# Optimization experiments

Measured on AMD Instinct MI355X. Metric: run time of the kernel, lower is better.

The kernel has to match this reference:

```python
import jax, jax.numpy as jnp
import numpy as np

N_NODES = 50000
N_EDGES = 800000
D_IN = 96
D_OUT = 96
N_GRAPHS = 50


def setup_inputs() -> dict:
    key = jax.random.key(0)
    ks = jax.random.split(key, 16)
    s = 1.0 / np.sqrt(D_IN)
    inp = {
        "x": jax.random.normal(ks[0], (N_NODES, D_IN), jnp.float32),
        "edge_index": jax.random.randint(ks[1], (2, N_EDGES), 0, N_NODES, jnp.int32),
        "edge_attr": jax.random.uniform(ks[2], (N_EDGES, 1), jnp.float32),
        "batch": jnp.sort(jax.random.randint(ks[3], (N_NODES,), 0, N_GRAPHS, jnp.int32)),
        "w1_w": jax.random.normal(ks[4], (D_IN, D_OUT), jnp.float32) * s,
        "w1_b": jax.random.normal(ks[5], (D_OUT,), jnp.float32) * 0.01,
        "w2_w": jax.random.normal(ks[6], (D_IN, D_OUT), jnp.float32) * s,
        "w2_b": jax.random.normal(ks[7], (D_OUT,), jnp.float32) * 0.01,
        "w3_w": jax.random.normal(ks[8], (D_IN, D_OUT), jnp.float32) * s,
        "w3_b": jax.random.normal(ks[9], (D_OUT,), jnp.float32) * 0.01,
        "w4_w": jax.random.normal(ks[10], (D_IN, D_OUT), jnp.float32) * s,
        "w4_b": jax.random.normal(ks[11], (D_OUT,), jnp.float32) * 0.01,
        "w5_w": jax.random.normal(ks[12], (1, D_OUT), jnp.float32),
        "w5_b": jax.random.normal(ks[13], (D_OUT,), jnp.float32) * 0.01,
    }
    return inp


def reference(x, edge_index, edge_attr, batch,
              w1_w, w1_b, w2_w, w2_b, w3_w, w3_b, w4_w, w4_b, w5_w, w5_b):
    n = x.shape[0]
    src, dst = edge_index[0], edge_index[1]  # x_j = x[src], x_i = x[dst]
    sqrt_d = jnp.sqrt(jnp.asarray(D_OUT, x.dtype))

    x_i = x[dst]                                  # [E, D]
    x_j = x[src]                                  # [E, D]
    xi_t = x_i @ w3_w + w3_b                      # w3(x_i)
    xj_t = x_j @ w4_w + w4_b                      # w4(x_j)
    ea_t = edge_attr @ w5_w + w5_b                # w5(edge_attr), [E, D]

    scores = jnp.sum(xi_t * (xj_t + ea_t), axis=-1) / sqrt_d  # [E]

    # segment softmax over destination-node neighborhoods (PyG softmax)
    seg_max = jax.ops.segment_max(scores, dst, num_segments=n)
    ex = jnp.exp(scores - seg_max[dst])
    denom = jax.ops.segment_sum(ex, dst, num_segments=n)
    alpha = ex / (denom[dst] + jnp.asarray(1e-16, x.dtype))

    msg = alpha[:, None] * (x_j @ w2_w + w2_b)    # [E, D]
    aggr = jax.ops.segment_sum(msg, dst, num_segments=n)

    node_out = x @ w1_w + w1_b + aggr             # update: w1(x) + aggr

    # global mean pool per graph
    sums = jax.ops.segment_sum(node_out, batch, num_segments=N_GRAPHS)
    counts = jax.ops.segment_sum(jnp.ones((n,), x.dtype), batch, num_segments=N_GRAPHS)
    return sums / jnp.maximum(counts, 1.0)[:, None]
```

## Files before the change

### kernel.cpp

```cpp
#include <hip/hip_runtime.h>
#include <math.h>

#define D 96
#define RSQ 0.10206207261596577f
#define TSTRIDE 104

typedef __attribute__((ext_vector_type(8))) short short8;
typedef __attribute__((ext_vector_type(4))) float f32x4;

__device__ __forceinline__ unsigned short f2bf(float f){
  unsigned u = __float_as_uint(f);
  unsigned r = (u + 0x7fff + ((u >> 16) & 1)) >> 16;
  return (unsigned short)r;
}
__device__ __forceinline__ float bf2f(unsigned short h){
  return __uint_as_float(((unsigned)h) << 16);
}
__device__ __forceinline__ float bflo(unsigned u){ return __uint_as_float(u << 16); }
__device__ __forceinline__ float bfhi(unsigned u){ return __uint_as_float(u & 0xffff0000u); }
__device__ __forceinline__ int lbound(const int* __restrict__ a, int n, int v){
  int lo = 0, hi = n;
  while (lo < hi){ int mid = (lo + hi) >> 1; if (a[mid] < v) lo = mid + 1; else hi = mid; }
  return lo;
}

__global__ __launch_bounds__(256) void k_wprep(
    const float* __restrict__ w1, const float* __restrict__ w2,
    const float* __restrict__ w3, const float* __restrict__ w4,
    unsigned short* __restrict__ wt_h, unsigned short* __restrict__ wt_l){
  int idx = blockIdx.x * 256 + threadIdx.x;
  if (idx >= 4 * D * D) return;
  int m = idx / (D * D);
  int r = idx % (D * D);
  int nn = r / D, k = r % D;
  const float* w = (m == 0) ? w1 : (m == 1) ? w2 : (m == 2) ? w3 : w4;
  float v = w[k * D + nn];
  unsigned short h = f2bf(v);
  wt_h[idx] = h;
  wt_l[idx] = f2bf(v - bf2f(h));
}

__global__ __launch_bounds__(256) void k_transform_mfma(
    const float* __restrict__ x,
    const unsigned short* __restrict__ wt_h, const unsigned short* __restrict__ wt_l,
    const float* __restrict__ b1, const float* __restrict__ b2,
    const float* __restrict__ b3, const float* __restrict__ b4,
    const float* __restrict__ w5, const float* __restrict__ b5,
    float* __restrict__ acc_o, unsigned short* __restrict__ x2o,
    float* __restrict__ x3o, unsigned short* __restrict__ x4o,
    float* __restrict__ p5, float* __restrict__ pb, int n){
  __shared__ __align__(16) unsigned short xs_h[16][TSTRIDE];
  __shared__ __align__(16) unsigned short xs_l[16][TSTRIDE];
  int tid = threadIdx.x;
  int n0 = blockIdx.x * 16;
  for (int e = tid; e < 16 * D; e += 256){
    int r = e / D, c = e % D;
    int node = n0 + r;
    float v = (node < n) ? x[(size_t)node * D + c] : 0.0f;
    unsigned short h = f2bf(v);
    xs_h[r][c] = h;
    xs_l[r][c] = f2bf(v - bf2f(h));
  }
  __syncthreads();

  int wv = tid >> 6;
  int lane = tid & 63;
  int lr = lane & 15;
  int kg = lane >> 4;

  f32x4 acc0 = {0,0,0,0}, acc1 = {0,0,0,0}, acc2 = {0,0,0,0};
  f32x4 acc3 = {0,0,0,0}, acc4 = {0,0,0,0}, acc5 = {0,0,0,0};
  const unsigned short* wtm_h = wt_h + (size_t)wv * D * D;
  const unsigned short* wtm_l = wt_l + (size_t)wv * D * D;

  #pragma unroll
  for (int k0 = 0; k0 < D; k0 += 32){
    int kb = k0 + kg * 8;
    short8 ah = *(const short8*)&xs_h[lr][kb];
    short8 al = *(const short8*)&xs_l[lr][kb];
    #pragma unroll
    for (int nc = 0; nc < 6; ++nc){
      int col = nc * 16 + lr;
      short8 bh = *(const short8*)(wtm_h + col * D + kb);
      short8 bl = *(const short8*)(wtm_l + col * D + kb);
      f32x4 a = (nc == 0) ? acc0 : (nc == 1) ? acc1 : (nc == 2) ? acc2
              : (nc == 3) ? acc3 : (nc == 4) ? acc4 : acc5;
      a = __builtin_amdgcn_mfma_f32_16x16x32_bf16(ah, bh, a, 0, 0, 0);
      a = __builtin_amdgcn_mfma_f32_16x16x32_bf16(ah, bl, a, 0, 0, 0);
      a = __builtin_amdgcn_mfma_f32_16x16x32_bf16(al, bh, a, 0, 0, 0);
      if (nc == 0) acc0 = a; else if (nc == 1) acc1 = a; else if (nc == 2) acc2 = a;
      else if (nc == 3) acc3 = a; else if (nc == 4) acc4 = a; else acc5 = a;
    }
  }

  const float* bias = (wv == 0) ? b1 : (wv == 1) ? b2 : (wv == 2) ? b3 : b4;
  float p5p0 = 0, p5p1 = 0, p5p2 = 0, p5p3 = 0;
  float pbp0 = 0, pbp1 = 0, pbp2 = 0, pbp3 = 0;
  #pragma unroll
  for (int nc = 0; nc < 6; ++nc){
    int col = nc * 16 + lr;
    float bb = bias[col];
    float w5v = w5[col], b5v = b5[col];
    f32x4 a = (nc == 0) ? acc0 : (nc == 1) ? acc1 : (nc == 2) ? acc2
            : (nc == 3) ? acc3 : (nc == 4) ? acc4 : acc5;
    #pragma unroll
    for (int q = 0; q < 4; ++q){
      float v = a[q] + bb;
      int row = kg * 4 + q;
      if (n0 + row < n){
        size_t o = (size_t)(n0 + row) * D + col;
        if (wv == 0) acc_o[o] = v;
        else if (wv == 1) x2o[o] = f2bf(v);
        else if (wv == 2) x3o[o] = v;
        else x4o[o] = f2bf(v);
      }
      float t5 = v * w5v, tb = v * b5v;
      if (q == 0){ p5p0 += t5; pbp0 += tb; }
      else if (q == 1){ p5p1 += t5; pbp1 += tb; }
      else if (q == 2){ p5p2 += t5; pbp2 += tb; }
      else { p5p3 += t5; pbp3 += tb; }
    }
  }
  if (wv == 2){
    #pragma unroll
    for (int off = 1; off < 16; off <<= 1){
      p5p0 += __shfl_xor(p5p0, off); pbp0 += __shfl_xor(pbp0, off);
      p5p1 += __shfl_xor(p5p1, off); pbp1 += __shfl_xor(pbp1, off);
      p5p2 += __shfl_xor(p5p2, off); pbp2 += __shfl_xor(pbp2, off);
      p5p3 += __shfl_xor(p5p3, off); pbp3 += __shfl_xor(pbp3, off);
    }
    if (lr == 0){
      int row = kg * 4;
      if (n0 + row < n)     { p5[n0 + row]     = p5p0; pb[n0 + row]     = pbp0; }
      if (n0 + row + 1 < n) { p5[n0 + row + 1] = p5p1; pb[n0 + row + 1] = pbp1; }
      if (n0 + row + 2 < n) { p5[n0 + row + 2] = p5p2; pb[n0 + row + 2] = pbp2; }
      if (n0 + row + 3 < n) { p5[n0 + row + 3] = p5p3; pb[n0 + row + 3] = pbp3; }
    }
  }
}

__global__ __launch_bounds__(256) void k_deg(
    const int* __restrict__ dstI, int* __restrict__ deg, int E){
  int e = blockIdx.x * blockDim.x + threadIdx.x;
  if (e >= E) return;
  atomicAdd(&deg[dstI[e]], 1);
}

__global__ __launch_bounds__(256) void k_scanA(
    const int* __restrict__ deg, int* __restrict__ rowp,
    int* __restrict__ partials, int n){
  __shared__ int ws[4];
  int tid = threadIdx.x, lane = tid & 63, wid = tid >> 6;
  int i = blockIdx.x * 256 + tid;
  int v = (i < n) ? deg[i] : 0;
  int s = v;
  #pragma unroll
  for (int off = 1; off < 64; off <<= 1){ int u = __shfl_up(s, off); if (lane >= off) s += u; }
  if (lane == 63) ws[wid] = s;
  __syncthreads();
  if (tid < 4){
    int u = ws[tid];
    #pragma unroll
    for (int off = 1; off < 4; off <<= 1){ int q = __shfl_up(u, off); if (tid >= off) u += q; }
    ws[tid] = u;
  }
  __syncthreads();
  int woff = wid ? ws[wid - 1] : 0;
  if (i < n) rowp[i] = woff + s - v;
  if (tid == 255) partials[blockIdx.x] = ws[3];
}

__global__ __launch_bounds__(256) void k_scanB(
    int* __restrict__ partials, int* __restrict__ rowp, int nb, int n){
  __shared__ int ws[4];
  int tid = threadIdx.x, lane = tid & 63, wid = tid >> 6;
  int running = 0;
  for (int base = 0; base < nb; base += 256){
    int i = base + tid;
    int v = (i < nb) ? partials[i] : 0;
    int s = v;
    #pragma unroll
    for (int off = 1; off < 64; off <<= 1){ int u = __shfl_up(s, off); if (lane >= off) s += u; }
    if (lane == 63) ws[wid] = s;
    __syncthreads();
    if (tid < 4){
      int u = ws[tid];
      #pragma unroll
      for (int off = 1; off < 4; off <<= 1){ int q = __shfl_up(u, off); if (tid >= off) u += q; }
      ws[tid] = u;
    }
    __syncthreads();
    int woff = wid ? ws[wid - 1] : 0;
    if (i < nb) partials[i] = running + woff + s - v;
    running += ws[3];
    __syncthreads();
  }
  if (tid == 0) rowp[n] = running;
}

__global__ __launch_bounds__(256) void k_scatter(
    const int* __restrict__ srcI, const int* __restrict__ dstI,
    const float* __restrict__ eattr, const int* __restrict__ rowp,
    const int* __restrict__ partials, int* __restrict__ fill,
    int2* __restrict__ sortedSE, int E){
  int e = blockIdx.x * blockDim.x + threadIdx.x;
  if (e >= E) return;
  int t = dstI[e];
  int pos = rowp[t] + partials[t >> 8] + atomicAdd(&fill[t], 1);
  sortedSE[pos] = make_int2(srcI[e], __float_as_int(eattr[e]));
}

__global__ __launch_bounds__(256) void k_attn(
    const unsigned short* __restrict__ x2b, const float* __restrict__ x3,
    const unsigned short* __restrict__ x4b, const float* __restrict__ p5,
    const float* __restrict__ pb, const int2* __restrict__ sortedSE,
    const int* __restrict__ rowp, const int* __restrict__ partials,
    float* __restrict__ node_acc, int n){
  int t = blockIdx.x * 4 + (threadIdx.x >> 6);
  int lane = threadIdx.x & 63;
  if (t >= n) return;
  int beg = rowp[t] + partials[t >> 8];
  int end = (t + 1 < n) ? (rowp[t + 1] + partials[(t + 1) >> 8]) : rowp[n];
  if (beg == end) return;
  int j = lane & 15;

  const float2* r3 = (const float2*)(x3 + (size_t)t * D);
  float2 v0 = r3[j], v1 = r3[j + 16], v2 = r3[j + 32];
  float p5t = p5[t], pbt = pb[t];

  float m = -INFINITY, dsum = 0.0f;
  float a0 = 0, a1 = 0, a2 = 0, a3 = 0, a4 = 0, a5 = 0;

  for (int c = beg; c < end; c += 4){
    int g = lane >> 4;
    int ei = c + g;
    bool act = ei < end;
    int2 se = sortedSE[act ? ei : end - 1];
    const unsigned* r4 = (const unsigned*)(x4b + (size_t)se.x * D);
    unsigned u0 = r4[j], u1 = r4[j + 16], u2 = r4[j + 32];
    float s = v0.x * bflo(u0) + v0.y * bfhi(u0)
            + v1.x * bflo(u1) + v1.y * bfhi(u1)
            + v2.x * bflo(u2) + v2.y * bfhi(u2);
    s += __shfl_xor(s, 1); s += __shfl_xor(s, 2);
    s += __shfl_xor(s, 4); s += __shfl_xor(s, 8);
    float sc = act ? (s + __int_as_float(se.y) * p5t + pbt) * RSQ : -INFINITY;
    float mc = fmaxf(sc, __shfl_xor(sc, 16));
    mc = fmaxf(mc, __shfl_xor(mc, 32));
    if (mc > m){
      float r = __expf(m - mc);
      dsum *= r; a0 *= r; a1 *= r; a2 *= r; a3 *= r; a4 *= r; a5 *= r;
      m = mc;
    }
    float w = __expf(sc - m);
    dsum += w;
    const unsigned* r2 = (const unsigned*)(x2b + (size_t)se.x * D);
    unsigned q0 = r2[j], q1 = r2[j + 16], q2 = r2[j + 32];
    a0 += w * bflo(q0); a1 += w * bfhi(q0);
    a2 += w * bflo(q1); a3 += w * bfhi(q1);
    a4 += w * bflo(q2); a5 += w * bfhi(q2);
  }
  a0 += __shfl_xor(a0, 16); a0 += __shfl_xor(a0, 32);
  a1 += __shfl_xor(a1, 16); a1 += __shfl_xor(a1, 32);
  a2 += __shfl_xor(a2, 16); a2 += __shfl_xor(a2, 32);
  a3 += __shfl_xor(a3, 16); a3 += __shfl_xor(a3, 32);
  a4 += __shfl_xor(a4, 16); a4 += __shfl_xor(a4, 32);
  a5 += __shfl_xor(a5, 16); a5 += __shfl_xor(a5, 32);
  dsum += __shfl_xor(dsum, 16); dsum += __shfl_xor(dsum, 32);
  float inv = 1.0f / (dsum + 1e-16f);
  if (lane < 16){
    size_t o = (size_t)t * D + 2 * j;
    node_acc[o]      += a0 * inv;
    node_acc[o + 1]  += a1 * inv;
    node_acc[o + 32] += a2 * inv;
    node_acc[o + 33] += a3 * inv;
    node_acc[o + 64] += a4 * inv;
    node_acc[o + 65] += a5 * inv;
  }
}

__global__ __launch_bounds__(96) void k_pool(
    const float* __restrict__ node_out, const int* __restrict__ batch,
    float* __restrict__ sums, int n){
  int g = blockIdx.x;
  int chunk = blockIdx.y, nch = gridDim.y;
  int lo = lbound(batch, n, g);
  int hi = lbound(batch, n, g + 1);
  int cnt = hi - lo;
  if (cnt <= 0) return;
  int per = (cnt + nch - 1) / nch;
  int b = lo + chunk * per;
  int e = min(b + per, hi);
  if (b >= e) return;
  int d = threadIdx.x;
  float s = 0.0f;
  for (int r = b; r < e; ++r) s += node_out[(size_t)r * D + d];
  atomicAdd(&sums[g * D + d], s);
}

__global__ __launch_bounds__(256) void k_final(
    const float* __restrict__ sums, const int* __restrict__ batch,
    float* __restrict__ out, int n, int total){
  int i = blockIdx.x * blockDim.x + threadIdx.x;
  if (i >= total) return;
  int g = i / D;
  int lo = lbound(batch, n, g);
  int hi = lbound(batch, n, g + 1);
  float c = (float)((hi - lo) > 1 ? (hi - lo) : 1);
  out[i] = sums[i] / c;
}

extern "C" void kernel_launch(void* const* d_in, const int* in_sizes, int n_in,
                              void* d_out, int out_size, void* d_ws, size_t ws_size,
                              hipStream_t stream){
  const float* x     = (const float*)d_in[0];
  const int*   eidx  = (const int*)d_in[1];
  const float* eattr = (const float*)d_in[2];
  const int*   batch = (const int*)d_in[3];
  const float* w1 = (const float*)d_in[4];
  const float* b1 = (const float*)d_in[5];
  const float* w2 = (const float*)d_in[6];
  const float* b2 = (const float*)d_in[7];
  const float* w3 = (const float*)d_in[8];
  const float* b3 = (const float*)d_in[9];
  const float* w4 = (const float*)d_in[10];
  const float* b4 = (const float*)d_in[11];
  const float* w5 = (const float*)d_in[12];
  const float* b5 = (const float*)d_in[13];
  float* out = (float*)d_out;

  const int N = in_sizes[0] / D;
  const int E = in_sizes[2];
  const int* srcI = eidx;
  const int* dstI = eidx + E;
  const int NB = (N + 255) / 256;

  char* base = (char*)d_ws;
  size_t off = 0;
  auto alloc = [&](size_t bytes) -> char* {
    char* p = base + off;
    off = (off + bytes + 255) & ~(size_t)255;
    return p;
  };
  char* zbase = base;
  int*   deg  = (int*)alloc((size_t)N * 4);
  int*   fill = (int*)alloc((size_t)N * 4);
  float* sums = (float*)alloc((size_t)out_size * 4);
  size_t zbytes = off;
  float* node_acc = (float*)alloc((size_t)N * D * 4);
  unsigned short* x2v = (unsigned short*)alloc((size_t)N * D * 2);
  float* x3v      = (float*)alloc((size_t)N * D * 4);
  unsigned short* x4v = (unsigned short*)alloc((size_t)N * D * 2);
  float* p5       = (float*)alloc((size_t)N * 4);
  float* pb       = (float*)alloc((size_t)N * 4);
  int*   rowp     = (int*)alloc((size_t)(N + 1) * 4);
  int*   partials = (int*)alloc((size_t)(NB + 1) * 4);
  int2*  sortedSE = (int2*)alloc((size_t)E * 8);
  unsigned short* wt_h = (unsigned short*)alloc((size_t)4 * D * D * 2);
  unsigned short* wt_l = (unsigned short*)alloc((size_t)4 * D * D * 2);
  (void)ws_size; (void)n_in;

  hipMemsetAsync(zbase, 0, zbytes, stream);

  k_wprep<<<dim3((4 * D * D + 255) / 256), dim3(256), 0, stream>>>(
      w1, w2, w3, w4, wt_h, wt_l);
  k_transform_mfma<<<dim3((N + 15) / 16), dim3(256), 0, stream>>>(
      x, wt_h, wt_l, b1, b2, b3, b4, w5, b5,
      node_acc, x2v, x3v, x4v, p5, pb, N);
  k_deg<<<dim3((E + 255) / 256), dim3(256), 0, stream>>>(dstI, deg, E);
  k_scanA<<<dim3(NB), dim3(256), 0, stream>>>(deg, rowp, partials, N);
  k_scanB<<<dim3(1), dim3(256), 0, stream>>>(partials, rowp, NB, N);
  k_scatter<<<dim3((E + 255) / 256), dim3(256), 0, stream>>>(
      srcI, dstI, eattr, rowp, partials, fill, sortedSE, E);
  k_attn<<<dim3((N + 3) / 4), dim3(256), 0, stream>>>(
      x2v, x3v, x4v, p5, pb, sortedSE, rowp, partials, node_acc, N);
  k_pool<<<dim3(out_size / D, 32), dim3(D), 0, stream>>>(node_acc, batch, sums, N);
  k_final<<<dim3((out_size + 255) / 256), dim3(256), 0, stream>>>(
      sums, batch, out, N, out_size);
}
```

Measured before the change: 313.0 us.

## Fuse graph build into cooperative kernel, unroll attention by two, fuse pool finalize

The weight prep, degree count, node transform, prefix scans and edge scatter are merged into one cooperative persistent kernel that uses grid syncs in place of separate launches. If the cooperative launch fails, it falls back to separate kernels. The attention loop now handles two edges per lane group per iteration to raise memory-level parallelism. The final mean division moves into the pool kernel through a last-block-done counter. The aim is to cut launch overhead and raise gather throughput. The cost is that 512 persistent blocks can give lower occupancy for the transform and scatter phases, plus grid-sync overhead.

```diff
diff --git a/kernel.cpp b/kernel.cpp
--- a/kernel.cpp
+++ b/kernel.cpp
@@ -1,5 +1,8 @@
 #include <hip/hip_runtime.h>
+#include <hip/hip_cooperative_groups.h>
 #include <math.h>
+
+namespace cg = cooperative_groups;
 
 #define D 96
 #define RSQ 0.10206207261596577f
@@ -24,160 +27,135 @@
   return lo;
 }
 
-__global__ __launch_bounds__(256) void k_wprep(
-    const float* __restrict__ w1, const float* __restrict__ w2,
-    const float* __restrict__ w3, const float* __restrict__ w4,
-    unsigned short* __restrict__ wt_h, unsigned short* __restrict__ wt_l){
-  int idx = blockIdx.x * 256 + threadIdx.x;
-  if (idx >= 4 * D * D) return;
-  int m = idx / (D * D);
-  int r = idx % (D * D);
-  int nn = r / D, k = r % D;
-  const float* w = (m == 0) ? w1 : (m == 1) ? w2 : (m == 2) ? w3 : w4;
-  float v = w[k * D + nn];
-  unsigned short h = f2bf(v);
-  wt_h[idx] = h;
-  wt_l[idx] = f2bf(v - bf2f(h));
-}
-
-__global__ __launch_bounds__(256) void k_transform_mfma(
-    const float* __restrict__ x,
-    const unsigned short* __restrict__ wt_h, const unsigned short* __restrict__ wt_l,
-    const float* __restrict__ b1, const float* __restrict__ b2,
-    const float* __restrict__ b3, const float* __restrict__ b4,
-    const float* __restrict__ w5, const float* __restrict__ b5,
-    float* __restrict__ acc_o, unsigned short* __restrict__ x2o,
-    float* __restrict__ x3o, unsigned short* __restrict__ x4o,
-    float* __restrict__ p5, float* __restrict__ pb, int n){
-  __shared__ __align__(16) unsigned short xs_h[16][TSTRIDE];
-  __shared__ __align__(16) unsigned short xs_l[16][TSTRIDE];
+struct BuildArgs {
+  const float* x;
+  const float *w1, *b1, *w2, *b2, *w3, *b3, *w4, *b4, *w5, *b5;
+  const int *srcI, *dstI;
+  const float* eattr;
+  unsigned short *wt_h, *wt_l;
+  float* acc_o; unsigned short* x2o; float* x3o; unsigned short* x4o;
+  float *p5, *pb;
+  int *deg, *fill, *rowp, *partials;
+  int2* sortedSE;
+  int N, E, NB, NT;
+};
+
+
+__device__ __forceinline__ void do_wprep(const BuildArgs& A, int gtid, int gstride){
+  for (int idx = gtid; idx < 4 * D * D; idx += gstride){
+    int m = idx / (D * D);
+    int r = idx % (D * D);
+    int nn = r / D, k = r % D;
+    const float* w = (m == 0) ? A.w1 : (m == 1) ? A.w2 : (m == 2) ? A.w3 : A.w4;
+    float v = w[k * D + nn];
+    unsigned short h = f2bf(v);
+    A.wt_h[idx] = h;
+    A.wt_l[idx] = f2bf(v - bf2f(h));
+  }
+}
+
+__device__ __forceinline__ void do_deg(const BuildArgs& A, int gtid, int gstride){
+  for (int e = gtid; e < A.E; e += gstride) atomicAdd(&A.deg[A.dstI[e]], 1);
+}
+
+__device__ __forceinline__ void do_transform(const BuildArgs& A,
+    unsigned short (*xs_h)[TSTRIDE], unsigned short (*xs_l)[TSTRIDE],
+    int tile0, int tstride){
   int tid = threadIdx.x;
-  int n0 = blockIdx.x * 16;
-  for (int e = tid; e < 16 * D; e += 256){
-    int r = e / D, c = e % D;
-    int node = n0 + r;
-    float v = (node < n) ? x[(size_t)node * D + c] : 0.0f;
-    unsigned short h = f2bf(v);
-    xs_h[r][c] = h;
-    xs_l[r][c] = f2bf(v - bf2f(h));
-  }
-  __syncthreads();
-
+  int lane = tid & 63;
   int wv = tid >> 6;
-  int lane = tid & 63;
   int lr = lane & 15;
   int kg = lane >> 4;
-
-  f32x4 acc0 = {0,0,0,0}, acc1 = {0,0,0,0}, acc2 = {0,0,0,0};
-  f32x4 acc3 = {0,0,0,0}, acc4 = {0,0,0,0}, acc5 = {0,0,0,0};
-  const unsigned short* wtm_h = wt_h + (size_t)wv * D * D;
-  const unsigned short* wtm_l = wt_l + (size_t)wv * D * D;
-
-  #pragma unroll
-  for (int k0 = 0; k0 < D; k0 += 32){
-    int kb = k0 + kg * 8;
-    short8 ah = *(const short8*)&xs_h[lr][kb];
-    short8 al = *(const short8*)&xs_l[lr][kb];
+  const unsigned short* wtm_h = A.wt_h + (size_t)wv * D * D;
+  const unsigned short* wtm_l = A.wt_l + (size_t)wv * D * D;
+  const float* bias = (wv == 0) ? A.b1 : (wv == 1) ? A.b2 : (wv == 2) ? A.b3 : A.b4;
+  for (int tile = tile0; tile < A.NT; tile += tstride){
+    int n0 = tile * 16;
+    for (int e = tid; e < 16 * D; e += 256){
+      int r = e / D, c = e % D;
+      int node = n0 + r;
+      float v = (node < A.N) ? A.x[(size_t)node * D + c] : 0.0f;
+      unsigned short h = f2bf(v);
+      xs_h[r][c] = h;
+      xs_l[r][c] = f2bf(v - bf2f(h));
+    }
+    __syncthreads();
+
+    f32x4 acc0 = {0,0,0,0}, acc1 = {0,0,0,0}, acc2 = {0,0,0,0};
+    f32x4 acc3 = {0,0,0,0}, acc4 = {0,0,0,0}, acc5 = {0,0,0,0};
+    #pragma unroll
+    for (int k0 = 0; k0 < D; k0 += 32){
+      int kb = k0 + kg * 8;
+      short8 ah = *(const short8*)&xs_h[lr][kb];
+      short8 al = *(const short8*)&xs_l[lr][kb];
+      #pragma unroll
+      for (int nc = 0; nc < 6; ++nc){
+        int col = nc * 16 + lr;
+        short8 bh = *(const short8*)(wtm_h + col * D + kb);
+        short8 bl = *(const short8*)(wtm_l + col * D + kb);
+        f32x4 a = (nc == 0) ? acc0 : (nc == 1) ? acc1 : (nc == 2) ? acc2
+                : (nc == 3) ? acc3 : (nc == 4) ? acc4 : acc5;
+        a = __builtin_amdgcn_mfma_f32_16x16x32_bf16(ah, bh, a, 0, 0, 0);
+        a = __builtin_amdgcn_mfma_f32_16x16x32_bf16(ah, bl, a, 0, 0, 0);
+        a = __builtin_amdgcn_mfma_f32_16x16x32_bf16(al, bh, a, 0, 0, 0);
+        if (nc == 0) acc0 = a; else if (nc == 1) acc1 = a; else if (nc == 2) acc2 = a;
+        else if (nc == 3) acc3 = a; else if (nc == 4) acc4 = a; else acc5 = a;
+      }
+    }
+
+    float p5p0 = 0, p5p1 = 0, p5p2 = 0, p5p3 = 0;
+    float pbp0 = 0, pbp1 = 0, pbp2 = 0, pbp3 = 0;
     #pragma unroll
     for (int nc = 0; nc < 6; ++nc){
       int col = nc * 16 + lr;
-      short8 bh = *(const short8*)(wtm_h + col * D + kb);
-      short8 bl = *(const short8*)(wtm_l + col * D + kb);
+      float bb = bias[col];
+      float w5v = A.w5[col], b5v = A.b5[col];
       f32x4 a = (nc == 0) ? acc0 : (nc == 1) ? acc1 : (nc == 2) ? acc2
               : (nc == 3) ? acc3 : (nc == 4) ? acc4 : acc5;
-      a = __builtin_amdgcn_mfma_f32_16x16x32_bf16(ah, bh, a, 0, 0, 0);
-      a = __builtin_amdgcn_mfma_f32_16x16x32_bf16(ah, bl, a, 0, 0, 0);
-      a = __builtin_amdgcn_mfma_f32_16x16x32_bf16(al, bh, a, 0, 0, 0);
-      if (nc == 0) acc0 = a; else if (nc == 1) acc1 = a; else if (nc == 2) acc2 = a;
-      else if (nc == 3) acc3 = a; else if (nc == 4) acc4 = a; else acc5 = a;
-    }
-  }
-
-  const float* bias = (wv == 0) ? b1 : (wv == 1) ? b2 : (wv == 2) ? b3 : b4;
-  float p5p0 = 0, p5p1 = 0, p5p2 = 0, p5p3 = 0;
-  float pbp0 = 0, pbp1 = 0, pbp2 = 0, pbp3 = 0;
-  #pragma unroll
-  for (int nc = 0; nc < 6; ++nc){
-    int col = nc * 16 + lr;
-    float bb = bias[col];
-    float w5v = w5[col], b5v = b5[col];
-    f32x4 a = (nc == 0) ? acc0 : (nc == 1) ? acc1 : (nc == 2) ? acc2
-            : (nc == 3) ? acc3 : (nc == 4) ? acc4 : acc5;
-    #pragma unroll
-    for (int q = 0; q < 4; ++q){
-      float v = a[q] + bb;
-      int row = kg * 4 + q;
-      if (n0 + row < n){
-        size_t o = (size_t)(n0 + row) * D + col;
-        if (wv == 0) acc_o[o] = v;
-        else if (wv == 1) x2o[o] = f2bf(v);
-        else if (wv == 2) x3o[o] = v;
-        else x4o[o] = f2bf(v);
+      #pragma unroll
+      for (int q = 0; q < 4; ++q){
+        float v = a[q] + bb;
+        int row = kg * 4 + q;
+        if (n0 + row < A.N){
+          size_t o = (size_t)(n0 + row) * D + col;
+          if (wv == 0) A.acc_o[o] = v;
+          else if (wv == 1) A.x2o[o] = f2bf(v);
+          else if (wv == 2) A.x3o[o] = v;
+          else A.x4o[o] = f2bf(v);
+        }
+        float t5 = v * w5v, tb = v * b5v;
+        if (q == 0){ p5p0 += t5; pbp0 += tb; }
+        else if (q == 1){ p5p1 += t5; pbp1 += tb; }
+        else if (q == 2){ p5p2 += t5; pbp2 += tb; }
+        else { p5p3 += t5; pbp3 += tb; }
       }
-      float t5 = v * w5v, tb = v * b5v;
-      if (q == 0){ p5p0 += t5; pbp0 += tb; }
-      else if (q == 1){ p5p1 += t5; pbp1 += tb; }
-      else if (q == 2){ p5p2 += t5; pbp2 += tb; }
-      else { p5p3 += t5; pbp3 += tb; }
-    }
-  }
-  if (wv == 2){
-    #pragma unroll
-    for (int off = 1; off < 16; off <<= 1){
-      p5p0 += __shfl_xor(p5p0, off); pbp0 += __shfl_xor(pbp0, off);
-      p5p1 += __shfl_xor(p5p1, off); pbp1 += __shfl_xor(pbp1, off);
-      p5p2 += __shfl_xor(p5p2, off); pbp2 += __shfl_xor(pbp2, off);
-      p5p3 += __shfl_xor(p5p3, off); pbp3 += __shfl_xor(pbp3, off);
-    }
-    if (lr == 0){
-      int row = kg * 4;
-      if (n0 + row < n)     { p5[n0 + row]     = p5p0; pb[n0 + row]     = pbp0; }
-      if (n0 + row + 1 < n) { p5[n0 + row + 1] = p5p1; pb[n0 + row + 1] = pbp1; }
-      if (n0 + row + 2 < n) { p5[n0 + row + 2] = p5p2; pb[n0 + row + 2] = pbp2; }
-      if (n0 + row + 3 < n) { p5[n0 + row + 3] = p5p3; pb[n0 + row + 3] = pbp3; }
-    }
-  }
-}
-
-__global__ __launch_bounds__(256) void k_deg(
-    const int* __restrict__ dstI, int* __restrict__ deg, int E){
-  int e = blockIdx.x * blockDim.x + threadIdx.x;
-  if (e >= E) return;
-  atomicAdd(&deg[dstI[e]], 1);
-}
-
-__global__ __launch_bounds__(256) void k_scanA(
-    const int* __restrict__ deg, int* __restrict__ rowp,
-    int* __restrict__ partials, int n){
-  __shared__ int ws[4];
+    }
+    if (wv == 2){
+      #pragma unroll
+      for (int off = 1; off < 16; off <<= 1){
+        p5p0 += __shfl_xor(p5p0, off); pbp0 += __shfl_xor(pbp0, off);
+        p5p1 += __shfl_xor(p5p1, off); pbp1 += __shfl_xor(pbp1, off);
+        p5p2 += __shfl_xor(p5p2, off); pbp2 += __shfl_xor(pbp2, off);
+        p5p3 += __shfl_xor(p5p3, off); pbp3 += __shfl_xor(pbp3, off);
+      }
+      if (lr == 0){
+        int row = kg * 4;
+        if (n0 + row < A.N)     { A.p5[n0 + row]     = p5p0; A.pb[n0 + row]     = pbp0; }
+        if (n0 + row + 1 < A.N) { A.p5[n0 + row + 1] = p5p1; A.pb[n0 + row + 1] = pbp1; }
+        if (n0 + row + 2 < A.N) { A.p5[n0 + row + 2] = p5p2; A.pb[n0 + row + 2] = pbp2; }
+        if (n0 + row + 3 < A.N) { A.p5[n0 + row + 3] = p5p3; A.pb[n0 + row + 3] = pbp3; }
+      }
+    }
+    __syncthreads();
+  }
+}
+
+__device__ __forceinline__ void do_scanA(const BuildArgs& A, int* ws,
+                                         int chunk0, int cstride){
   int tid = threadIdx.x, lane = tid & 63, wid = tid >> 6;
-  int i = blockIdx.x * 256 + tid;
-  int v = (i < n) ? deg[i] : 0;
-  int s = v;
-  #pragma unroll
-  for (int off = 1; off < 64; off <<= 1){ int u = __shfl_up(s, off); if (lane >= off) s += u; }
-  if (lane == 63) ws[wid] = s;
-  __syncthreads();
-  if (tid < 4){
-    int u = ws[tid];
-    #pragma unroll
-    for (int off = 1; off < 4; off <<= 1){ int q = __shfl_up(u, off); if (tid >= off) u += q; }
-    ws[tid] = u;
-  }
-  __syncthreads();
-  int woff = wid ? ws[wid - 1] : 0;
-  if (i < n) rowp[i] = woff + s - v;
-  if (tid == 255) partials[blockIdx.x] = ws[3];
-}
-
-__global__ __launch_bounds__(256) void k_scanB(
-    int* __restrict__ partials, int* __restrict__ rowp, int nb, int n){
-  __shared__ int ws[4];
-  int tid = threadIdx.x, lane = tid & 63, wid = tid >> 6;
-  int running = 0;
-  for (int base = 0; base < nb; base += 256){
-    int i = base + tid;
-    int v = (i < nb) ? partials[i] : 0;
+  for (int chunk = chunk0; chunk < A.NB; chunk += cstride){
+    int i = chunk * 256 + tid;
+    int v = (i < A.N) ? A.deg[i] : 0;
     int s = v;
     #pragma unroll
     for (int off = 1; off < 64; off <<= 1){ int u = __shfl_up(s, off); if (lane >= off) s += u; }
@@ -191,23 +169,87 @@
     }
     __syncthreads();
     int woff = wid ? ws[wid - 1] : 0;
-    if (i < nb) partials[i] = running + woff + s - v;
+    if (i < A.N) A.rowp[i] = woff + s - v;
+    if (tid == 255) A.partials[chunk] = ws[3];
+    __syncthreads();
+  }
+}
+
+__device__ __forceinline__ void do_scanB(const BuildArgs& A, int* ws){
+  int tid = threadIdx.x, lane = tid & 63, wid = tid >> 6;
+  int running = 0;
+  for (int base = 0; base < A.NB; base += 256){
+    int i = base + tid;
+    int v = (i < A.NB) ? A.partials[i] : 0;
+    int s = v;
+    #pragma unroll
+    for (int off = 1; off < 64; off <<= 1){ int u = __shfl_up(s, off); if (lane >= off) s += u; }
+    if (lane == 63) ws[wid] = s;
+    __syncthreads();
+    if (tid < 4){
+      int u = ws[tid];
+      #pragma unroll
+      for (int off = 1; off < 4; off <<= 1){ int q = __shfl_up(u, off); if (tid >= off) u += q; }
+      ws[tid] = u;
+    }
+    __syncthreads();
+    int woff = wid ? ws[wid - 1] : 0;
+    if (i < A.NB) A.partials[i] = running + woff + s - v;
     running += ws[3];
     __syncthreads();
   }
-  if (tid == 0) rowp[n] = running;
-}
-
-__global__ __launch_bounds__(256) void k_scatter(
-    const int* __restrict__ srcI, const int* __restrict__ dstI,
-    const float* __restrict__ eattr, const int* __restrict__ rowp,
-    const int* __restrict__ partials, int* __restrict__ fill,
-    int2* __restrict__ sortedSE, int E){
-  int e = blockIdx.x * blockDim.x + threadIdx.x;
-  if (e >= E) return;
-  int t = dstI[e];
-  int pos = rowp[t] + partials[t >> 8] + atomicAdd(&fill[t], 1);
-  sortedSE[pos] = make_int2(srcI[e], __float_as_int(eattr[e]));
+  if (tid == 0) A.rowp[A.N] = running;
+}
+
+__device__ __forceinline__ void do_scatter(const BuildArgs& A, int gtid, int gstride){
+  for (int e = gtid; e < A.E; e += gstride){
+    int t = A.dstI[e];
+    int pos = A.rowp[t] + A.partials[t >> 8] + atomicAdd(&A.fill[t], 1);
+    A.sortedSE[pos] = make_int2(A.srcI[e], __float_as_int(A.eattr[e]));
+  }
+}
+
+__global__ __launch_bounds__(256, 2) void k_build(BuildArgs A){
+  cg::grid_group grid = cg::this_grid();
+  __shared__ __align__(16) unsigned short xs_h[16][TSTRIDE];
+  __shared__ __align__(16) unsigned short xs_l[16][TSTRIDE];
+  __shared__ int ws[4];
+  int tid = threadIdx.x;
+  int gtid = blockIdx.x * 256 + tid;
+  int gstride = gridDim.x * 256;
+
+  do_wprep(A, gtid, gstride);
+  do_deg(A, gtid, gstride);
+  grid.sync();
+  do_transform(A, xs_h, xs_l, blockIdx.x, gridDim.x);
+  do_scanA(A, ws, blockIdx.x, gridDim.x);
+  grid.sync();
+  if (blockIdx.x == 0) do_scanB(A, ws);
+  grid.sync();
+  do_scatter(A, gtid, gstride);
+}
+
+__global__ __launch_bounds__(256) void k_wprep_deg(BuildArgs A){
+  int gtid = blockIdx.x * 256 + threadIdx.x, gstride = gridDim.x * 256;
+  do_wprep(A, gtid, gstride);
+  do_deg(A, gtid, gstride);
+}
+__global__ __launch_bounds__(256) void k_transform_sep(BuildArgs A){
+  __shared__ __align__(16) unsigned short xs_h[16][TSTRIDE];
+  __shared__ __align__(16) unsigned short xs_l[16][TSTRIDE];
+  do_transform(A, xs_h, xs_l, blockIdx.x, gridDim.x);
+}
+__global__ __launch_bounds__(256) void k_scanA_sep(BuildArgs A){
+  __shared__ int ws[4];
+  do_scanA(A, ws, blockIdx.x, gridDim.x);
+}
+__global__ __launch_bounds__(256) void k_scanB_sep(BuildArgs A){
+  __shared__ int ws[4];
+  do_scanB(A, ws);
+}
+__global__ __launch_bounds__(256) void k_scatter_sep(BuildArgs A){
+  int gtid = blockIdx.x * 256 + threadIdx.x, gstride = gridDim.x * 256;
+  do_scatter(A, gtid, gstride);
 }
 
 __global__ __launch_bounds__(256) void k_attn(
@@ -223,6 +265,7 @@
   int end = (t + 1 < n) ? (rowp[t + 1] + partials[(t + 1) >> 8]) : rowp[n];
   if (beg == end) return;
   int j = lane & 15;
+  int g = lane >> 4;
 
   const float2* r3 = (const float2*)(x3 + (size_t)t * D);
   float2 v0 = r3[j], v1 = r3[j + 16], v2 = r3[j + 32];
@@ -231,33 +274,48 @@
   float m = -INFINITY, dsum = 0.0f;
   float a0 = 0, a1 = 0, a2 = 0, a3 = 0, a4 = 0, a5 = 0;
 
-  for (int c = beg; c < end; c += 4){
-    int g = lane >> 4;
-    int ei = c + g;
-    bool act = ei < end;
-    int2 se = sortedSE[act ? ei : end - 1];
-    const unsigned* r4 = (const unsigned*)(x4b + (size_t)se.x * D);
-    unsigned u0 = r4[j], u1 = r4[j + 16], u2 = r4[j + 32];
-    float s = v0.x * bflo(u0) + v0.y * bfhi(u0)
-            + v1.x * bflo(u1) + v1.y * bfhi(u1)
-            + v2.x * bflo(u2) + v2.y * bfhi(u2);
-    s += __shfl_xor(s, 1); s += __shfl_xor(s, 2);
-    s += __shfl_xor(s, 4); s += __shfl_xor(s, 8);
-    float sc = act ? (s + __int_as_float(se.y) * p5t + pbt) * RSQ : -INFINITY;
-    float mc = fmaxf(sc, __shfl_xor(sc, 16));
+  for (int c = beg; c < end; c += 8){
+    int eA = c + g, eB = c + 4 + g;
+    bool actA = eA < end, actB = eB < end;
+    int2 seA = sortedSE[actA ? eA : end - 1];
+    int2 seB = sortedSE[actB ? eB : end - 1];
+    const unsigned* r4A = (const unsigned*)(x4b + (size_t)seA.x * D);
+    const unsigned* r4B = (const unsigned*)(x4b + (size_t)seB.x * D);
+    unsigned uA0 = r4A[j], uA1 = r4A[j + 16], uA2 = r4A[j + 32];
+    unsigned uB0 = r4B[j], uB1 = r4B[j + 16], uB2 = r4B[j + 32];
+    float sA = v0.x * bflo(uA0) + v0.y * bfhi(uA0)
+             + v1.x * bflo(uA1) + v1.y * bfhi(uA1)
+             + v2.x * bflo(uA2) + v2.y * bfhi(uA2);
+    float sB = v0.x * bflo(uB0) + v0.y * bfhi(uB0)
+             + v1.x * bflo(uB1) + v1.y * bfhi(uB1)
+             + v2.x * bflo(uB2) + v2.y * bfhi(uB2);
+    sA += __shfl_xor(sA, 1); sA += __shfl_xor(sA, 2);
+    sA += __shfl_xor(sA, 4); sA += __shfl_xor(sA, 8);
+    sB += __shfl_xor(sB, 1); sB += __shfl_xor(sB, 2);
+    sB += __shfl_xor(sB, 4); sB += __shfl_xor(sB, 8);
+    float scA = actA ? (sA + __int_as_float(seA.y) * p5t + pbt) * RSQ : -INFINITY;
+    float scB = actB ? (sB + __int_as_float(seB.y) * p5t + pbt) * RSQ : -INFINITY;
+    float mc = fmaxf(scA, scB);
+    mc = fmaxf(mc, __shfl_xor(mc, 16));
     mc = fmaxf(mc, __shfl_xor(mc, 32));
     if (mc > m){
       float r = __expf(m - mc);
       dsum *= r; a0 *= r; a1 *= r; a2 *= r; a3 *= r; a4 *= r; a5 *= r;
       m = mc;
     }
-    float w = __expf(sc - m);
-    dsum += w;
-    const unsigned* r2 = (const unsigned*)(x2b + (size_t)se.x * D);
-    unsigned q0 = r2[j], q1 = r2[j + 16], q2 = r2[j + 32];
-    a0 += w * bflo(q0); a1 += w * bfhi(q0);
-    a2 += w * bflo(q1); a3 += w * bfhi(q1);
-    a4 += w * bflo(q2); a5 += w * bfhi(q2);
+    float wA = __expf(scA - m);
+    float wB = __expf(scB - m);
+    dsum += wA + wB;
+    const unsigned* r2A = (const unsigned*)(x2b + (size_t)seA.x * D);
+    const unsigned* r2B = (const unsigned*)(x2b + (size_t)seB.x * D);
+    unsigned qA0 = r2A[j], qA1 = r2A[j + 16], qA2 = r2A[j + 32];
+    unsigned qB0 = r2B[j], qB1 = r2B[j + 16], qB2 = r2B[j + 32];
+    a0 += wA * bflo(qA0) + wB * bflo(qB0);
+    a1 += wA * bfhi(qA0) + wB * bfhi(qB0);
+    a2 += wA * bflo(qA1) + wB * bflo(qB1);
+    a3 += wA * bfhi(qA1) + wB * bfhi(qB1);
+    a4 += wA * bflo(qA2) + wB * bflo(qB2);
+    a5 += wA * bfhi(qA2) + wB * bfhi(qB2);
   }
   a0 += __shfl_xor(a0, 16); a0 += __shfl_xor(a0, 32);
   a1 += __shfl_xor(a1, 16); a1 += __shfl_xor(a1, 32);
@@ -280,33 +338,31 @@
 
 __global__ __launch_bounds__(96) void k_pool(
     const float* __restrict__ node_out, const int* __restrict__ batch,
-    float* __restrict__ sums, int n){
+    float* __restrict__ sums, int* __restrict__ gdone,
+    float* __restrict__ out, int n){
   int g = blockIdx.x;
   int chunk = blockIdx.y, nch = gridDim.y;
+  int d = threadIdx.x;
   int lo = lbound(batch, n, g);
   int hi = lbound(batch, n, g + 1);
-  int cnt = hi - lo;
-  if (cnt <= 0) return;
-  int per = (cnt + nch - 1) / nch;
-  int b = lo + chunk * per;
-  int e = min(b + per, hi);
-  if (b >= e) return;
-  int d = threadIdx.x;
   float s = 0.0f;
-  for (int r = b; r < e; ++r) s += node_out[(size_t)r * D + d];
+  if (hi > lo){
+    int per = (hi - lo + nch - 1) / nch;
+    int b = lo + chunk * per;
+    int e = min(b + per, hi);
+    for (int r = b; r < e; ++r) s += node_out[(size_t)r * D + d];
+  }
   atomicAdd(&sums[g * D + d], s);
-}
-
-__global__ __launch_bounds__(256) void k_final(
-    const float* __restrict__ sums, const int* __restrict__ batch,
-    float* __restrict__ out, int n, int total){
-  int i = blockIdx.x * blockDim.x + threadIdx.x;
-  if (i >= total) return;
-  int g = i / D;
-  int lo = lbound(batch, n, g);
-  int hi = lbound(batch, n, g + 1);
-  float c = (float)((hi - lo) > 1 ? (hi - lo) : 1);
-  out[i] = sums[i] / c;
+  __threadfence();
+  __syncthreads();
+  __shared__ int tk;
+  if (d == 0) tk = atomicAdd(&gdone[g], 1);
+  __syncthreads();
+  if (tk == nch - 1){
+    float c = (float)((hi - lo) > 1 ? (hi - lo) : 1);
+    float v = atomicAdd(&sums[g * D + d], 0.0f);
+    out[g * D + d] = v / c;
+  }
 }
 
 extern "C" void kernel_launch(void* const* d_in, const int* in_sizes, int n_in,
@@ -333,6 +389,8 @@
   const int* srcI = eidx;
   const int* dstI = eidx + E;
   const int NB = (N + 255) / 256;
+  const int NT = (N + 15) / 16;
+  const int NG = out_size / D;
 
   char* base = (char*)d_ws;
   size_t off = 0;
@@ -342,9 +400,10 @@
     return p;
   };
   char* zbase = base;
-  int*   deg  = (int*)alloc((size_t)N * 4);
-  int*   fill = (int*)alloc((size_t)N * 4);
-  float* sums = (float*)alloc((size_t)out_size * 4);
+  int*   deg   = (int*)alloc((size_t)N * 4);
+  int*   fill  = (int*)alloc((size_t)N * 4);
+  float* sums  = (float*)alloc((size_t)out_size * 4);
+  int*   gdone = (int*)alloc((size_t)NG * 4);
   size_t zbytes = off;
   float* node_acc = (float*)alloc((size_t)N * D * 4);
   unsigned short* x2v = (unsigned short*)alloc((size_t)N * D * 2);
@@ -361,19 +420,32 @@
 
   hipMemsetAsync(zbase, 0, zbytes, stream);
 
-  k_wprep<<<dim3((4 * D * D + 255) / 256), dim3(256), 0, stream>>>(
-      w1, w2, w3, w4, wt_h, wt_l);
-  k_transform_mfma<<<dim3((N + 15) / 16), dim3(256), 0, stream>>>(
-      x, wt_h, wt_l, b1, b2, b3, b4, w5, b5,
-      node_acc, x2v, x3v, x4v, p5, pb, N);
-  k_deg<<<dim3((E + 255) / 256), dim3(256), 0, stream>>>(dstI, deg, E);
-  k_scanA<<<dim3(NB), dim3(256), 0, stream>>>(deg, rowp, partials, N);
-  k_scanB<<<dim3(1), dim3(256), 0, stream>>>(partials, rowp, NB, N);
-  k_scatter<<<dim3((E + 255) / 256), dim3(256), 0, stream>>>(
-      srcI, dstI, eattr, rowp, partials, fill, sortedSE, E);
+  BuildArgs A;
+  A.x = x;
+  A.w1 = w1; A.b1 = b1; A.w2 = w2; A.b2 = b2;
+  A.w3 = w3; A.b3 = b3; A.w4 = w4; A.b4 = b4;
+  A.w5 = w5; A.b5 = b5;
+  A.srcI = srcI; A.dstI = dstI; A.eattr = eattr;
+  A.wt_h = wt_h; A.wt_l = wt_l;
+  A.acc_o = node_acc; A.x2o = x2v; A.x3o = x3v; A.x4o = x4v;
+  A.p5 = p5; A.pb = pb;
+  A.deg = deg; A.fill = fill; A.rowp = rowp; A.partials = partials;
+  A.sortedSE = sortedSE;
+  A.N = N; A.E = E; A.NB = NB; A.NT = NT;
+
+  void* kargs[] = { &A };
+  hipError_t cerr = hipLaunchCooperativeKernel((const void*)k_build, dim3(512),
+                                               dim3(256), kargs, 0, stream);
+  if (cerr != hipSuccess){
+    k_wprep_deg<<<dim3((E + 255) / 256), dim3(256), 0, stream>>>(A);
+    k_transform_sep<<<dim3(NT), dim3(256), 0, stream>>>(A);
+    k_scanA_sep<<<dim3(NB), dim3(256), 0, stream>>>(A);
+    k_scanB_sep<<<dim3(1), dim3(256), 0, stream>>>(A);
+    k_scatter_sep<<<dim3((E + 255) / 256), dim3(256), 0, stream>>>(A);
+  }
+
   k_attn<<<dim3((N + 3) / 4), dim3(256), 0, stream>>>(
       x2v, x3v, x4v, p5, pb, sortedSE, rowp, partials, node_acc, N);
-  k_pool<<<dim3(out_size / D, 32), dim3(D), 0, stream>>>(node_acc, batch, sums, N);
-  k_final<<<dim3((out_size + 255) / 256), dim3(256), 0, stream>>>(
-      sums, batch, out, N, out_size);
-}
+  k_pool<<<dim3(NG, 32), dim3(D), 0, stream>>>(
+      node_acc, batch, sums, gdone, out, N);
+}
```

Result: slower. 568.5 us (+81.6%).
